# Kernel tuning notes

Measured on AMD Instinct MI355X. Metric: run time of the kernel, lower is better.

## Reference

```python
import jax, jax.numpy as jnp
import numpy as np

NUM_CLASSES = 20
FC = 512  # feature_channels
H = W = 28


def _conv(x, w, b):
    y = jax.lax.conv_general_dilated(x, w, (1, 1), 'SAME',
                                     dimension_numbers=('NCHW', 'OIHW', 'NCHW'))
    return y + b[None, :, None, None]


def _center_map(centers, height, width):
    # centers: [B, N, 4] = (x, y, class, conf); vectorized scatter replacing the python loop
    B, N, _ = centers.shape
    xp = (centers[..., 0] * width).astype(jnp.int32)   # int() truncation; x>=0 so == floor
    yp = (centers[..., 1] * height).astype(jnp.int32)
    conf = centers[..., 3]
    valid = (xp >= 0) & (xp < width) & (yp >= 0) & (yp < height)
    flat = jnp.where(valid, yp * width + xp, height * width)  # invalid -> dummy slot
    m = jnp.zeros((B, height * width + 1), centers.dtype)
    m = m.at[jnp.arange(B)[:, None], flat].set(conf)
    return m[:, :height * width].reshape(B, 1, height, width)


def setup_inputs() -> dict:
    key = jax.random.key(0)
    ks = jax.random.split(key, 16)
    B = 256
    image = jax.random.normal(ks[0], (B, 3, H, W), jnp.float32)
    features = jax.random.normal(ks[1], (B, FC, 7, 7), jnp.float32)
    centers = jax.random.uniform(ks[2], (B, 100, 4), jnp.float32)

    def conv_w(k, co, ci):
        s = 1.0 / np.sqrt(ci * 9)
        return jax.random.uniform(k, (co, ci, 3, 3), jnp.float32, -s, s)

    def lin_w(k, co, ci):
        s = 1.0 / np.sqrt(ci)
        return jax.random.uniform(k, (co, ci), jnp.float32, -s, s)

    cin = FC + 3 + 1  # 516
    return {
        'image': image, 'features': features, 'centers': centers,
        'w1': conv_w(ks[3], 128, cin), 'b1': jnp.zeros((128,), jnp.float32),
        'w2': conv_w(ks[4], 64, 128), 'b2': jnp.zeros((64,), jnp.float32),
        'w3': conv_w(ks[5], 32, 64), 'b3': jnp.zeros((32,), jnp.float32),
        'w4': conv_w(ks[6], 16, 32), 'b4': jnp.zeros((16,), jnp.float32),
        'fw1': lin_w(ks[7], 256, 16 * H * W), 'fb1': jnp.zeros((256,), jnp.float32),
        'fw2': lin_w(ks[8], 4 + NUM_CLASSES, 256), 'fb2': jnp.zeros((4 + NUM_CLASSES,), jnp.float32),
    }


def reference(image, features, centers, w1, b1, w2, b2, w3, b3, w4, b4, fw1, fb1, fw2, fb2):
    B = image.shape[0]
    feats = jax.image.resize(features, (B, FC, H, W), method='bilinear')  # align_corners=False
    cmap = _center_map(centers, H, W)
    x = jnp.concatenate([image, feats, cmap], axis=1)  # [B, 516, 28, 28]
    x = jax.nn.relu(_conv(x, w1, b1))
    x = jax.nn.relu(_conv(x, w2, b2))
    x = jax.nn.relu(_conv(x, w3, b3))
    x = jax.nn.relu(_conv(x, w4, b4))
    x = x.reshape(B, -1)
    x = jax.nn.relu(x @ fw1.T + fb1)
    action = x @ fw2.T + fb2  # [B, 4 + num_classes]
    action = action.at[:, 2].set(jax.nn.sigmoid(action[:, 2]))
    action = action.at[:, 3].set(jax.nn.sigmoid(action[:, 3]))
    return action
```

## Files before the change

### kernel.cpp

```cpp
#include <hip/hip_runtime.h>

typedef _Float16 f16;
typedef _Float16 f16x8 __attribute__((ext_vector_type(8)));
typedef float    f32x4 __attribute__((ext_vector_type(4)));

static __device__ __forceinline__ f16x8 ld8(const f16* p) {
    return *reinterpret_cast<const f16x8*>(p);
}

static constexpr size_t W1T_B  = 1253376;
static constexpr size_t W2T_B  = 147456;
static constexpr size_t W3T_B  = 36864;
static constexpr size_t W4T_B  = 9216;
static constexpr size_t FW1T_B = 6422528;
static constexpr size_t WEIGHTS_B = W1T_B + W2T_B + W3T_B + W4T_B + FW1T_B;

static constexpr size_t PB_X0 = 979200;
static constexpr size_t PB_X1 = 230400;
static constexpr size_t PB_X2 = 115200;
static constexpr size_t PB_X3 = 57600;
static constexpr size_t PB_X4 = 25088;
static constexpr size_t PB_X5 = 512;
static constexpr size_t PER_BATCH = PB_X0 + PB_X1 + PB_X2 + PB_X3 + PB_X4 + PB_X5;

static __device__ __forceinline__ void wxf(const float* __restrict__ w, f16* __restrict__ wt,
                                           int i, int CINr, int NCB, int COUT) {
    int co = i % COUT;
    int r  = i / COUT;
    int hi = r & 3; r >>= 2;
    int cb = r % NCB;
    int tap = r / NCB;
    f16x8 v;
    #pragma unroll
    for (int j = 0; j < 8; ++j) {
        int ci = cb * 32 + hi * 8 + j;
        float x = (ci < CINr) ? w[((size_t)co * CINr + ci) * 9 + tap] : 0.f;
        v[j] = (f16)x;
    }
    *reinterpret_cast<f16x8*>(wt + (size_t)i * 8) = v;
}

static constexpr int S1 = 9 * 17 * 4 * 128;
static constexpr int S2 = 9 * 4  * 4 * 64;
static constexpr int S3 = 9 * 2  * 4 * 32;
static constexpr int S4 = 9 * 1  * 4 * 16;
static constexpr int SW = S1 + S2 + S3 + S4;
static constexpr int SFW = 256 * 12544;
static constexpr int PREP_TOT = SW + SFW;

__global__ void prep_all(const float* __restrict__ w1, const float* __restrict__ w2,
                         const float* __restrict__ w3, const float* __restrict__ w4,
                         const float* __restrict__ fw1,
                         f16* __restrict__ W1t, f16* __restrict__ W2t,
                         f16* __restrict__ W3t, f16* __restrict__ W4t,
                         f16* __restrict__ FW1t) {
    int t = blockIdx.x * 256 + threadIdx.x;
    if (t >= PREP_TOT) return;
    if (t < S1) { wxf(w1, W1t, t, 516, 17, 128); return; }
    t -= S1;
    if (t < S2) { wxf(w2, W2t, t, 128, 4, 64); return; }
    t -= S2;
    if (t < S3) { wxf(w3, W3t, t, 64, 2, 32); return; }
    t -= S3;
    if (t < S4) { wxf(w4, W4t, t, 32, 1, 16); return; }
    t -= S4;
    int o = t / 12544, idx = t % 12544;
    int y = idx / 448, rem = idx % 448;
    int x = rem / 16, c = rem & 15;
    FW1t[t] = (f16)fw1[(size_t)o * 12544 + c * 784 + y * 28 + x];
}

static __device__ __forceinline__ void ring_yx(int bi, int& y, int& x) {
    if (bi < 30)      { y = 0;        x = bi; }
    else if (bi < 60) { y = 29;       x = bi - 30; }
    else if (bi < 88) { y = bi - 59;  x = 0; }
    else              { y = bi - 87;  x = 29; }
}

__global__ __launch_bounds__(512) void build_x0(
        const float* __restrict__ img, const float* __restrict__ feat,
        const float* __restrict__ centers,
        f16* __restrict__ X0, f16* __restrict__ X1,
        f16* __restrict__ X2, f16* __restrict__ X3, int b0) {
    const int bl = blockIdx.x;
    const int b  = b0 + bl;
    const int tid = threadIdx.x;
    f16* x0b = X0 + (size_t)bl * (17 * 900 * 32);

    for (int i = tid; i < 116 * 544; i += 512) {
        int c = i % 544, bi = i / 544;
        int y, x; ring_yx(bi, y, x);
        x0b[((size_t)(c >> 5) * 900 + y * 30 + x) * 32 + (c & 31)] = (f16)0.f;
    }
    for (int i = tid; i < 784; i += 512) {
        int y = i / 28, x = i % 28;
        x0b[((size_t)16 * 900 + (y + 1) * 30 + x + 1) * 32 + 3] = (f16)0.f;
    }
    for (int i = tid; i < 3 * 784; i += 512) {
        int c = i / 784, p = i % 784;
        int y = p / 28, x = p % 28;
        x0b[((size_t)(y + 1) * 30 + x + 1) * 32 + c] =
            (f16)img[((size_t)b * 3 + c) * 784 + p];
    }
    {
        const int c  = tid + 3;
        const int cb = c >> 5, c32 = c & 31;
        const float* fb = feat + ((size_t)b * 512 + tid) * 49;
        float r0[7], r1[7];
        int cur = -100;
        for (int y = 0; y < 28; ++y) {
            float sy = (y + 0.5f) * 0.25f - 0.5f;
            float fy = floorf(sy);
            int iy0 = (int)fy;
            float wy1 = sy - fy, wy0 = 1.f - wy1;
            if (iy0 != cur) {
                cur = iy0;
                int i0 = iy0 < 0 ? 0 : iy0;
                int i1 = (iy0 + 1 > 6) ? 6 : iy0 + 1;
                #pragma unroll
                for (int j = 0; j < 7; ++j) { r0[j] = fb[i0 * 7 + j]; r1[j] = fb[i1 * 7 + j]; }
            }
            f16* orow = x0b + ((size_t)cb * 900 + (y + 1) * 30 + 1) * 32 + c32;
            #pragma unroll 28
            for (int x = 0; x < 28; ++x) {
                float sx = (x + 0.5f) * 0.25f - 0.5f;
                float fx = floorf(sx);
                int ix0 = (int)fx;
                float wx1 = sx - fx, wx0 = 1.f - wx1;
                int j0 = ix0 < 0 ? 0 : ix0;
                int j1 = (ix0 + 1 > 6) ? 6 : ix0 + 1;
                float v = wy0 * (wx0 * r0[j0] + wx1 * r0[j1]) +
                          wy1 * (wx0 * r1[j0] + wx1 * r1[j1]);
                orow[(size_t)x * 32] = (f16)v;
            }
        }
    }
    {
        f16* x1b = X1 + (size_t)bl * (4 * 900 * 32);
        for (int i = tid; i < 116 * 128; i += 512) {
            int c = i % 128, bi = i / 128;
            int y, x; ring_yx(bi, y, x);
            x1b[((size_t)(c >> 5) * 900 + y * 30 + x) * 32 + (c & 31)] = (f16)0.f;
        }
        f16* x2b = X2 + (size_t)bl * (2 * 900 * 32);
        for (int i = tid; i < 116 * 64; i += 512) {
            int c = i % 64, bi = i / 64;
            int y, x; ring_yx(bi, y, x);
            x2b[((size_t)(c >> 5) * 900 + y * 30 + x) * 32 + (c & 31)] = (f16)0.f;
        }
        f16* x3b = X3 + (size_t)bl * (900 * 32);
        for (int i = tid; i < 116 * 32; i += 512) {
            int c = i % 32, bi = i / 32;
            int y, x; ring_yx(bi, y, x);
            x3b[((size_t)y * 30 + x) * 32 + c] = (f16)0.f;
        }
    }
    __syncthreads();
    if (tid == 0) {
        const float* cb = centers + (size_t)b * 400;
        for (int n = 0; n < 100; ++n) {
            float cx = cb[n * 4 + 0], cy = cb[n * 4 + 1], conf = cb[n * 4 + 3];
            int xp = (int)(cx * 28.f);
            int yp = (int)(cy * 28.f);
            if (xp >= 0 && xp < 28 && yp >= 0 && yp < 28)
                x0b[((size_t)16 * 900 + (yp + 1) * 30 + xp + 1) * 32 + 3] = (f16)conf;
        }
    }
}

template<int CIN, int COUT, int GM, int GN, int WNT, int MW, bool PADOUT>
__global__ __launch_bounds__(512) void conv3x3(const f16* __restrict__ Xin,
                                               const f16* __restrict__ Wt,
                                               const float* __restrict__ bias,
                                               f16* __restrict__ Xout) {
    constexpr int NCB  = CIN / 32;
    constexpr int NCBO = COUT / 32;
    constexpr int NV_B = 9 * 4 * COUT;
    constexpr int PT   = (NV_B + 511) / 512;
    __shared__ f16 Bs[NV_B * 8];

    const int rg = blockIdx.x;
    const int b  = blockIdx.y;
    const int tid = threadIdx.x;
    const int wave = tid >> 6;
    const int lane = tid & 63;
    const int lm = lane & 15, hi = lane >> 4;
    const int wm = wave % GM, wn = wave / GM;
    const int MT = (rg < 3) ? 14 : 7;

    f32x4 acc[MW][WNT];
    #pragma unroll
    for (int k = 0; k < MW; ++k)
        #pragma unroll
        for (int n = 0; n < WNT; ++n)
            acc[k][n] = (f32x4){0.f, 0.f, 0.f, 0.f};

    const size_t bbase = (size_t)b * NCB * 900;
    int inoff[MW];
    #pragma unroll
    for (int k = 0; k < MW; ++k) {
        const int m = wm + k * GM;
        const int p = m * 16 + lm;
        const int yl = p / 28, x = p - yl * 28;
        inoff[k] = (m < MT) ? ((rg * 8 + yl) * 30 + x) : 0;
    }

    for (int cb = 0; cb < NCB; ++cb) {
        #pragma unroll
        for (int pi = 0; pi < PT; ++pi) {
            const int v = tid + pi * 512;
            if (v < NV_B) {
                const int tap = v / (4 * COUT);
                const int w   = v - tap * (4 * COUT);
                const f16* gsrc = Wt + ((size_t)(tap * NCB + cb) * (4 * COUT) + w) * 8;
                f16* ldst = Bs + (size_t)(pi * 512 + (tid & ~63)) * 8;
                __builtin_amdgcn_global_load_lds(
                    (const __attribute__((address_space(1))) void*)gsrc,
                    (__attribute__((address_space(3))) void*)ldst, 16, 0, 0);
            }
        }
        __syncthreads();

        #pragma unroll
        for (int tap = 0; tap < 9; ++tap) {
            f16x8 bf[WNT];
            #pragma unroll
            for (int n = 0; n < WNT; ++n)
                bf[n] = *reinterpret_cast<const f16x8*>(
                    Bs + ((size_t)(tap * 4 + hi) * COUT + (wn * WNT + n) * 16 + lm) * 8);
            const int dy = tap / 3, dx = tap - dy * 3;
            const size_t dOff = (bbase + (size_t)cb * 900 + dy * 30 + dx) * 32 + hi * 8;
            #pragma unroll
            for (int k = 0; k < MW; ++k) {
                if (wm + k * GM < MT) {
                    const f16x8 af = ld8(Xin + dOff + (size_t)inoff[k] * 32);
                    #pragma unroll
                    for (int n = 0; n < WNT; ++n)
                        acc[k][n] = __builtin_amdgcn_mfma_f32_16x16x32_f16(af, bf[n], acc[k][n], 0, 0, 0);
                }
            }
        }
        __syncthreads();
    }

    #pragma unroll
    for (int k = 0; k < MW; ++k) {
        const int m = wm + k * GM;
        if (m < MT) {
            #pragma unroll
            for (int n = 0; n < WNT; ++n) {
                const int co = (wn * WNT + n) * 16 + lm;
                const float bv = bias[co];
                #pragma unroll
                for (int r = 0; r < 4; ++r) {
                    const int p = m * 16 + hi * 4 + r;
                    const int yl = p / 28, x = p - yl * 28;
                    const float v = fmaxf(acc[k][n][r] + bv, 0.f);
                    size_t off;
                    if (PADOUT)
                        off = (((size_t)b * NCBO + (co >> 5)) * 900 +
                               (rg * 8 + yl + 1) * 30 + (x + 1)) * 32 + (co & 31);
                    else
                        off = ((size_t)b * 784 + (rg * 8 + yl) * 28 + x) * COUT + co;
                    Xout[off] = (f16)v;
                }
            }
        }
    }
}

__global__ __launch_bounds__(256) void fc1k(const f16* __restrict__ X4,
                                            const f16* __restrict__ FW1t,
                                            const float* __restrict__ fb1,
                                            f16* __restrict__ X5, int CH) {
    const int bm = blockIdx.x;
    const int nt = blockIdx.y * 4 + (threadIdx.x >> 6);
    const int lane = threadIdx.x & 63;
    const int lm = lane & 15, hi = lane >> 4;
    f32x4 acc = (f32x4){0.f, 0.f, 0.f, 0.f};
    const int row0 = bm * 16 + lm;
    const int rowA = (row0 < CH) ? row0 : 0;
    const f16* arow = X4 + (size_t)rowA * 12544;
    const int o = nt * 16 + lm;
    const f16* brow = FW1t + (size_t)o * 12544;
    for (int kk = 0; kk < 12544; kk += 32) {
        const f16x8 af = ld8(arow + kk + hi * 8);
        const f16x8 bf = ld8(brow + kk + hi * 8);
        acc = __builtin_amdgcn_mfma_f32_16x16x32_f16(af, bf, acc, 0, 0, 0);
    }
    const float bv = fb1[o];
    #pragma unroll
    for (int r = 0; r < 4; ++r) {
        const int row = bm * 16 + hi * 4 + r;
        if (row < CH)
            X5[(size_t)row * 256 + o] = (f16)fmaxf(acc[r] + bv, 0.f);
    }
}

__global__ void fc2k(const f16* __restrict__ X5, const float* __restrict__ fw2,
                     const float* __restrict__ fb2, float* __restrict__ out, int CH) {
    int t = blockIdx.x * 256 + threadIdx.x;
    if (t < CH * 24) {
        int b = t / 24, o = t % 24;
        float s = fb2[o];
        const f16* xr = X5 + (size_t)b * 256;
        const float* wr = fw2 + (size_t)o * 256;
        for (int k = 0; k < 256; ++k) s += (float)xr[k] * wr[k];
        if (o == 2 || o == 3) s = 1.f / (1.f + expf(-s));
        out[t] = s;
    }
}

extern "C" void kernel_launch(void* const* d_in, const int* in_sizes, int n_in,
                              void* d_out, int out_size, void* d_ws, size_t ws_size,
                              hipStream_t stream) {
    const float* image    = (const float*)d_in[0];
    const float* features = (const float*)d_in[1];
    const float* centers  = (const float*)d_in[2];
    const float* w1  = (const float*)d_in[3];
    const float* b1  = (const float*)d_in[4];
    const float* w2  = (const float*)d_in[5];
    const float* b2  = (const float*)d_in[6];
    const float* w3  = (const float*)d_in[7];
    const float* b3  = (const float*)d_in[8];
    const float* w4  = (const float*)d_in[9];
    const float* b4  = (const float*)d_in[10];
    const float* fw1 = (const float*)d_in[11];
    const float* fb1 = (const float*)d_in[12];
    const float* fw2 = (const float*)d_in[13];
    const float* fb2 = (const float*)d_in[14];

    int CH = 8;
    for (int c = 256; c >= 8; c >>= 1) {
        if (WEIGHTS_B + (size_t)c * PER_BATCH <= ws_size) { CH = c; break; }
    }

    char* ws = (char*)d_ws;
    f16* W1t  = (f16*)(ws);
    f16* W2t  = (f16*)(ws + W1T_B);
    f16* W3t  = (f16*)(ws + W1T_B + W2T_B);
    f16* W4t  = (f16*)(ws + W1T_B + W2T_B + W3T_B);
    f16* FW1t = (f16*)(ws + W1T_B + W2T_B + W3T_B + W4T_B);
    char* act = ws + WEIGHTS_B;
    f16* X0 = (f16*)(act);
    f16* X1 = (f16*)(act + (size_t)CH * PB_X0);
    f16* X2 = (f16*)(act + (size_t)CH * (PB_X0 + PB_X1));
    f16* X3 = (f16*)(act + (size_t)CH * (PB_X0 + PB_X1 + PB_X2));
    f16* X4 = (f16*)(act + (size_t)CH * (PB_X0 + PB_X1 + PB_X2 + PB_X3));
    f16* X5 = (f16*)(act + (size_t)CH * (PB_X0 + PB_X1 + PB_X2 + PB_X3 + PB_X4));

    prep_all<<<(PREP_TOT + 255) / 256, 256, 0, stream>>>(w1, w2, w3, w4, fw1,
                                                         W1t, W2t, W3t, W4t, FW1t);

    for (int b0 = 0; b0 < 256; b0 += CH) {
        build_x0<<<CH, 512, 0, stream>>>(image, features, centers,
                                         X0, X1, X2, X3, b0);

        dim3 cgrid(4, CH);
        conv3x3<544, 128, 4, 2, 4, 4, true ><<<cgrid, 512, 0, stream>>>(X0, W1t, b1, X1);
        conv3x3<128, 64,  4, 2, 2, 4, true ><<<cgrid, 512, 0, stream>>>(X1, W2t, b2, X2);
        conv3x3<64,  32,  4, 2, 1, 4, true ><<<cgrid, 512, 0, stream>>>(X2, W3t, b3, X3);
        conv3x3<32,  16,  8, 1, 1, 2, false><<<cgrid, 512, 0, stream>>>(X3, W4t, b4, X4);

        dim3 fgrid((CH + 15) / 16, 4);
        fc1k<<<fgrid, 256, 0, stream>>>(X4, FW1t, fb1, X5, CH);
        fc2k<<<(CH * 24 + 255) / 256, 256, 0, stream>>>(X5, fw2, fb2,
                                                        (float*)d_out + (size_t)b0 * 24, CH);
    }
}
```

Baseline: 838.0 us.

## Use 32x32x16 MFMA kernel for first conv with reordered weight layout

```diff
diff --git a/kernel.cpp b/kernel.cpp
--- a/kernel.cpp
+++ b/kernel.cpp
@@ -3,6 +3,7 @@
 typedef _Float16 f16;
 typedef _Float16 f16x8 __attribute__((ext_vector_type(8)));
 typedef float    f32x4 __attribute__((ext_vector_type(4)));
+typedef float    f32x16 __attribute__((ext_vector_type(16)));
 
 static __device__ __forceinline__ f16x8 ld8(const f16* p) {
     return *reinterpret_cast<const f16x8*>(p);
@@ -40,6 +41,24 @@
     *reinterpret_cast<f16x8*>(wt + (size_t)i * 8) = v;
 }
 
+static __device__ __forceinline__ void wxf32(const float* __restrict__ w,
+                                             f16* __restrict__ wt, int i) {
+    int co = i % 128;
+    int r  = i / 128;
+    int g  = r & 1; r >>= 1;
+    int kh = r & 1; r >>= 1;
+    int cb = r % 17;
+    int tap = r / 17;
+    f16x8 v;
+    #pragma unroll
+    for (int j = 0; j < 8; ++j) {
+        int ci = cb * 32 + kh * 16 + g * 8 + j;
+        float x = (ci < 516) ? w[((size_t)co * 516 + ci) * 9 + tap] : 0.f;
+        v[j] = (f16)x;
+    }
+    *reinterpret_cast<f16x8*>(wt + (size_t)i * 8) = v;
+}
+
 static constexpr int S1 = 9 * 17 * 4 * 128;
 static constexpr int S2 = 9 * 4  * 4 * 64;
 static constexpr int S3 = 9 * 2  * 4 * 32;
@@ -56,7 +75,7 @@
                          f16* __restrict__ FW1t) {
     int t = blockIdx.x * 256 + threadIdx.x;
     if (t >= PREP_TOT) return;
-    if (t < S1) { wxf(w1, W1t, t, 516, 17, 128); return; }
+    if (t < S1) { wxf32(w1, W1t, t); return; }
     t -= S1;
     if (t < S2) { wxf(w2, W2t, t, 128, 4, 64); return; }
     t -= S2;
@@ -164,6 +183,89 @@
             int yp = (int)(cy * 28.f);
             if (xp >= 0 && xp < 28 && yp >= 0 && yp < 28)
                 x0b[((size_t)16 * 900 + (yp + 1) * 30 + xp + 1) * 32 + 3] = (f16)conf;
+        }
+    }
+}
+
+__global__ __launch_bounds__(448) void conv1_32(const f16* __restrict__ Xin,
+                                                const f16* __restrict__ Wt,
+                                                const float* __restrict__ bias,
+                                                f16* __restrict__ Xout) {
+    constexpr int NCB  = 17;
+    constexpr int NV_B = 9 * 4 * 128;
+    constexpr int PT   = (NV_B + 447) / 448;
+    __shared__ f16 Bs[NV_B * 8];
+
+    const int rg = blockIdx.x;
+    const int b  = blockIdx.y;
+    const int tid = threadIdx.x;
+    const int w  = tid >> 6;
+    const int lane = tid & 63;
+    const int lr = lane & 31;
+    const int g  = lane >> 5;
+    const int PV = ((rg < 3) ? 8 : 4) * 28;
+    const int p  = w * 32 + lr;
+    const int pc = (p < PV) ? p : 0;
+    const int yl = pc / 28, xx = pc - yl * 28;
+    const int pixoff = (rg * 8 + yl) * 30 + xx;
+
+    f32x16 acc[4];
+    #pragma unroll
+    for (int n = 0; n < 4; ++n)
+        #pragma unroll
+        for (int r = 0; r < 16; ++r) acc[n][r] = 0.f;
+
+    const size_t bbase = (size_t)b * NCB * 900;
+
+    for (int cb = 0; cb < NCB; ++cb) {
+        #pragma unroll
+        for (int pi = 0; pi < PT; ++pi) {
+            const int v = tid + pi * 448;
+            if (v < NV_B) {
+                const int tap = v / 512;
+                const int w2  = v - tap * 512;
+                const f16* gsrc = Wt + ((size_t)(tap * NCB + cb) * 512 + w2) * 8;
+                f16* ldst = Bs + (size_t)(pi * 448 + (tid & ~63)) * 8;
+                __builtin_amdgcn_global_load_lds(
+                    (const __attribute__((address_space(1))) void*)gsrc,
+                    (__attribute__((address_space(3))) void*)ldst, 16, 0, 0);
+            }
+        }
+        __syncthreads();
+
+        #pragma unroll
+        for (int tap = 0; tap < 9; ++tap) {
+            const int dy = tap / 3, dx = tap - dy * 3;
+            const size_t abase = (bbase + (size_t)cb * 900 + pixoff + dy * 30 + dx) * 32 + g * 8;
+            const f16x8 a0 = ld8(Xin + abase);
+            const f16x8 a1 = ld8(Xin + abase + 16);
+            #pragma unroll
+            for (int n = 0; n < 4; ++n) {
+                const f16x8 b0 = *reinterpret_cast<const f16x8*>(
+                    Bs + ((size_t)(tap * 512 + 0 * 256 + g * 128) + n * 32 + lr) * 8);
+                const f16x8 b1 = *reinterpret_cast<const f16x8*>(
+                    Bs + ((size_t)(tap * 512 + 1 * 256 + g * 128) + n * 32 + lr) * 8);
+                acc[n] = __builtin_amdgcn_mfma_f32_32x32x16_f16(a0, b0, acc[n], 0, 0, 0);
+                acc[n] = __builtin_amdgcn_mfma_f32_32x32x16_f16(a1, b1, acc[n], 0, 0, 0);
+            }
+        }
+        __syncthreads();
+    }
+
+    #pragma unroll
+    for (int n = 0; n < 4; ++n) {
+        const int co = n * 32 + lr;
+        const float bv = bias[co];
+        #pragma unroll
+        for (int r = 0; r < 16; ++r) {
+            const int row = (r & 3) + 8 * (r >> 2) + 4 * g;
+            const int pp = w * 32 + row;
+            if (pp < PV) {
+                const int yy = pp / 28, xo = pp - yy * 28;
+                const size_t off = (((size_t)b * 4 + (co >> 5)) * 900 +
+                                    (rg * 8 + yy + 1) * 30 + (xo + 1)) * 32 + (co & 31);
+                Xout[off] = (f16)fmaxf(acc[n][r] + bv, 0.f);
+            }
         }
     }
 }
@@ -357,7 +459,7 @@
                                          X0, X1, X2, X3, b0);
 
         dim3 cgrid(4, CH);
-        conv3x3<544, 128, 4, 2, 4, 4, true ><<<cgrid, 512, 0, stream>>>(X0, W1t, b1, X1);
+        conv1_32<<<cgrid, 448, 0, stream>>>(X0, W1t, b1, X1);
         conv3x3<128, 64,  4, 2, 2, 4, true ><<<cgrid, 512, 0, stream>>>(X1, W2t, b2, X2);
         conv3x3<64,  32,  4, 2, 1, 4, true ><<<cgrid, 512, 0, stream>>>(X2, W3t, b3, X3);
         conv3x3<32,  16,  8, 1, 1, 2, false><<<cgrid, 512, 0, stream>>>(X3, W4t, b4, X4);
```

Result: faster. 772.9 us (-7.8%).
